# Kernel optimization log

Measured on AMD Instinct MI355X. Metric: run time of the kernel, lower is better.

Reference implementation:

```python
import jax, jax.numpy as jnp
import numpy as np

B, A, HR = 2, 180, 512
H_OUT = W_OUT = 512


def setup_inputs() -> dict:
    key = jax.random.key(0)
    k1, = jax.random.split(key, 1)
    sino = jax.random.normal(k1, (B, A, HR), dtype=jnp.float32)
    angles_deg = jnp.linspace(0.0, 180.0, A, endpoint=False, dtype=jnp.float32)
    return {"sino": sino, "angles_deg": angles_deg, "H": H_OUT, "W": W_OUT}


def _forward(sino, angles_deg, H, W):
    Bn, An, Hr = sino.shape
    pad = int(1.0 * 0.1 * min(H, W))  # pad_ratio = 1.0
    Hp, Wp = H + 2 * pad, W + 2 * pad

    # --- F.interpolate bilinear, align_corners=False: (A,B,Hr,1) -> (A,B,Hp,Wp).
    # Input width is 1, so width interp replicates the single column; only height interp matters.
    src = jnp.clip((jnp.arange(Hp, dtype=jnp.float32) + 0.5) * (Hr / Hp) - 0.5, 0.0, Hr - 1)
    i0 = jnp.floor(src).astype(jnp.int32)
    i1 = jnp.minimum(i0 + 1, Hr - 1)
    wH = src - i0.astype(jnp.float32)
    p = jnp.transpose(sino, (1, 0, 2)).astype(jnp.float32)  # (A,B,Hr)
    col = p[:, :, i0] * (1.0 - wH) + p[:, :, i1] * wH       # (A,B,Hp)
    proj = jnp.broadcast_to(col[:, :, :, None], (An, Bn, Hp, Wp))  # (A,B,Hp,Wp)

    # --- affine_grid (align_corners=False), sign = -1
    th = -jnp.deg2rad(angles_deg)
    c, s = jnp.cos(th), jnp.sin(th)                          # (A,)
    xs = (jnp.arange(Wp, dtype=jnp.float32) + 0.5) * (2.0 / Wp) - 1.0
    ys = (jnp.arange(Hp, dtype=jnp.float32) + 0.5) * (2.0 / Hp) - 1.0
    gx = c[:, None, None] * xs[None, None, :] - s[:, None, None] * ys[None, :, None]  # (A,Hp,Wp)
    gy = s[:, None, None] * xs[None, None, :] + c[:, None, None] * ys[None, :, None]

    # --- grid_sample bilinear, zeros padding, align_corners=False
    ix = ((gx + 1.0) * Wp - 1.0) * 0.5
    iy = ((gy + 1.0) * Hp - 1.0) * 0.5
    x0 = jnp.floor(ix).astype(jnp.int32); x1 = x0 + 1
    y0 = jnp.floor(iy).astype(jnp.int32); y1 = y0 + 1
    wx = ix - x0.astype(jnp.float32)
    wy = iy - y0.astype(jnp.float32)

    def corner(img, xi, yi, w):  # img (B,Hp,Wp); idx/w (Hp,Wp)
        valid = (xi >= 0) & (xi <= Wp - 1) & (yi >= 0) & (yi <= Hp - 1)
        xc = jnp.clip(xi, 0, Wp - 1)
        yc = jnp.clip(yi, 0, Hp - 1)
        return img[:, yc, xc] * (w * valid.astype(jnp.float32))[None]

    def sample(img, x0a, x1a, y0a, y1a, wxa, wya):
        return (corner(img, x0a, y0a, (1 - wxa) * (1 - wya)) +
                corner(img, x1a, y0a, wxa * (1 - wya)) +
                corner(img, x0a, y1a, (1 - wxa) * wya) +
                corner(img, x1a, y1a, wxa * wya))

    xr = jax.vmap(sample)(proj, x0, x1, y0, y1, wx, wy)      # (A,B,Hp,Wp)
    acc = xr.sum(axis=0) / (An + 1e-06)                      # (B,Hp,Wp)
    acc = acc[:, None, :, :]                                 # (B,1,Hp,Wp)
    if pad > 0:
        acc = acc[:, :, pad:Hp - pad, pad:Wp - pad]
    return acc


def reference(sino, angles_deg, H, W):
    return _forward(sino, angles_deg, H, W)
```

## Files before the change

kernel.cpp:

```cpp
#include <hip/hip_runtime.h>
#include <hip/hip_fp16.h>
#include <math.h>

#define B_N   2
#define A_N   180
#define HR_N  512
#define H_OUT 512
#define W_OUT 512
#define PAD   51
#define HP    614
#define WP    614
#define GUARD 80
#define HPP   (HP + 2*GUARD)
#define NPIX  (H_OUT * W_OUT)

#define TILE  16
#define QA    45
#define WIN   24


__device__ __forceinline__ float col_val(const float* __restrict__ sino,
                                         int b, int a, int yy) {
    if (yy < 0 || yy >= HP) return 0.0f;
    float src = ((float)yy + 0.5f) * ((float)HR_N / (float)HP) - 0.5f;
    src = fminf(fmaxf(src, 0.0f), (float)(HR_N - 1));
    int i0 = (int)floorf(src);
    int i1 = min(i0 + 1, HR_N - 1);
    float wH = src - (float)i0;
    const float* srow = sino + ((size_t)b * A_N + a) * HR_N;
    return srow[i0] * (1.0f - wH) + srow[i1] * wH;
}

__global__ void prep_kernel(const float* __restrict__ sino,
                            const float* __restrict__ angles,
                            uint2* __restrict__ pk2,
                            float2* __restrict__ tg) {
    int idx = blockIdx.x * blockDim.x + threadIdx.x;
    if (idx < A_N) {
        float th = -angles[idx] * (float)(M_PI / 180.0);
        tg[idx] = make_float2(cosf(th), sinf(th));
    }
    const int total = A_N * HPP;
    if (idx < total) {
        int y = idx % HPP;
        int a = idx / HPP;
        int yy = y - GUARD;
        float v00 = col_val(sino, 0, a, yy);
        float v10 = col_val(sino, 1, a, yy);
        float v01 = col_val(sino, 0, a, yy + 1);
        float v11 = col_val(sino, 1, a, yy + 1);
        __half2 lo = __floats2half2_rn(v00, v10);
        __half2 hi = __floats2half2_rn(v01, v11);
        uint2 u;
        u.x = *(unsigned int*)&lo;
        u.y = *(unsigned int*)&hi;
        pk2[idx] = u;
    }
}

__global__ __launch_bounds__(256, 4) void bp_kernel(const uint2* __restrict__ pk2,
                                                    const float2* __restrict__ tgv,
                                                    float* __restrict__ out) {
    __shared__ float2 s_tg[A_N];
    __shared__ int    s_base[A_N];
    __shared__ uint2  s_win[A_N * WIN];

    int t  = threadIdx.x;
    int tx = blockIdx.x, ty = blockIdx.y;
    float Xc = (float)(tx * TILE) - 248.0f;
    float Yc = (float)(ty * TILE) - 248.0f;

    if (t < A_N) {
        float2 cs = tgv[t];
        s_tg[t] = cs;
        float iyc = fmaf(cs.y, Xc, fmaf(cs.x, Yc, 306.5f));
        s_base[t] = (int)floorf(iyc) - 11;
    }
    __syncthreads();

    for (int e = t; e < A_N * WIN; e += 256) {
        int wid = e / WIN;
        int j   = e - wid * WIN;
        s_win[e] = pk2[(size_t)wid * HPP + (GUARD + s_base[wid] + j)];
    }
    __syncthreads();

    int q    = t >> 6;
    int lane = t & 63;
    int xq   = lane & 3;
    int yy   = lane >> 2;
    int x0   = tx * TILE + xq * 4;
    int y0   = ty * TILE + yy;
    float X  = (float)x0 - 255.5f;
    float Y  = (float)y0 - 255.5f;

    float2 acc[4] = {{0,0},{0,0},{0,0},{0,0}};

    bool interior = (Xc * Xc + Yc * Yc) <= 87500.0f;
    const int abase = q * QA;
    const uint2* winq = s_win + abase * WIN;

    if (interior) {
#pragma unroll 5
        for (int la = 0; la < QA; ++la) {
            float2 cs = s_tg[abase + la];
            float c = cs.x, s = cs.y;
            float iyc = fmaf(s, Xc, fmaf(c, Yc, 306.5f));
            float Kf  = 317.5f - floorf(iyc);
            float f0  = fmaf(s, X, fmaf(c, Y, Kf));
            float f1 = f0 + s, f2 = f1 + s, f3 = f2 + s;
            float fg[4] = {f0, f1, f2, f3};
#pragma unroll
            for (int g = 0; g < 4; ++g) {
                int   li = (int)fg[g];
                float wy = fg[g] - (float)li;
                uint2 cv = winq[la * WIN + li];
                __half2 lo = *(__half2*)&cv.x;
                __half2 hi = *(__half2*)&cv.y;
                __half2 r2 = __hfma2(__float2half2_rn(wy), __hsub2(hi, lo), lo);
                acc[g].x += __low2float(r2);
                acc[g].y += __high2float(r2);
            }
        }
    } else {
#pragma unroll 5
        for (int la = 0; la < QA; ++la) {
            float2 cs = s_tg[abase + la];
            float c = cs.x, s = cs.y;
            float iyc = fmaf(s, Xc, fmaf(c, Yc, 306.5f));
            float Kf  = 317.5f - floorf(iyc);
            float f0  = fmaf(s, X, fmaf(c, Y, Kf));
            float ix0 = fmaf(c, X, fmaf(-s, Y, 306.5f));
            float fg = f0, ixg = ix0;
#pragma unroll
            for (int g = 0; g < 4; ++g) {
                int   li = (int)fg;
                float wy = fg - (float)li;
                uint2 cv = winq[la * WIN + li];
                __half2 lo = *(__half2*)&cv.x;
                __half2 hi = *(__half2*)&cv.y;
                __half2 r2 = __hfma2(__float2half2_rn(wy), __hsub2(hi, lo), lo);
                float xf = fminf(fmaxf(ixg + 1.0f, 0.0f), 1.0f)
                         * fminf(fmaxf((float)WP - ixg, 0.0f), 1.0f);
                acc[g].x = fmaf(xf, __low2float(r2),  acc[g].x);
                acc[g].y = fmaf(xf, __high2float(r2), acc[g].y);
                fg += s; ixg += c;
            }
        }
    }

    __syncthreads();
    float* red = (float*)s_win;
    int px = yy * TILE + xq * 4;
    if (q != 0) {
        int o = (q - 1) * 512;
#pragma unroll
        for (int g = 0; g < 4; ++g) {
            red[o + px + g]       = acc[g].x;
            red[o + 256 + px + g] = acc[g].y;
        }
    }
    __syncthreads();
    if (q == 0) {
        const float inv = 1.0f / (180.0f + 1e-6f);
        float4 r0, r1;
        float* p0 = &r0.x; float* p1 = &r1.x;
#pragma unroll
        for (int g = 0; g < 4; ++g) {
            p0[g] = (acc[g].x + red[px + g]       + red[512 + px + g]       + red[1024 + px + g])       * inv;
            p1[g] = (acc[g].y + red[256 + px + g] + red[512 + 256 + px + g] + red[1024 + 256 + px + g]) * inv;
        }
        int idx = y0 * W_OUT + x0;
        *(float4*)&out[idx]        = r0;
        *(float4*)&out[NPIX + idx] = r1;
    }
}

extern "C" void kernel_launch(void* const* d_in, const int* in_sizes, int n_in,
                              void* d_out, int out_size, void* d_ws, size_t ws_size,
                              hipStream_t stream) {
    const float* sino   = (const float*)d_in[0];
    const float* angles = (const float*)d_in[1];
    char*   ws  = (char*)d_ws;
    uint2*  pk2 = (uint2*)ws;
    float2* tg  = (float2*)(ws + (size_t)A_N * HPP * sizeof(uint2));

    const int total = A_N * HPP;
    prep_kernel<<<(total + 255) / 256, 256, 0, stream>>>(sino, angles, pk2, tg);

    dim3 grid(W_OUT / TILE, H_OUT / TILE);
    bp_kernel<<<grid, 256, 0, stream>>>(pk2, tg, (float*)d_out);
}
```

Measured before the change: 84.91 us.

## Fuse projection prep into backprojection and accumulate interior tiles in half2

Drops the separate prep kernel. Each backprojection block now computes its own cos/sin table and fills its shared-memory window by interpolating the sinogram directly from global memory, so the launch and the workspace round trip go away. The cost is redundant interpolation and trig work in every block. Interior tiles also accumulate the 45 per-quarter samples in half2 rather than float, which saves conversions and adds but loses precision in the sums.

```diff
diff --git a/kernel.cpp b/kernel.cpp
--- a/kernel.cpp
+++ b/kernel.cpp
@@ -2,16 +2,12 @@
 #include <hip/hip_fp16.h>
 #include <math.h>
 
-#define B_N   2
 #define A_N   180
 #define HR_N  512
 #define H_OUT 512
 #define W_OUT 512
-#define PAD   51
 #define HP    614
 #define WP    614
-#define GUARD 80
-#define HPP   (HP + 2*GUARD)
 #define NPIX  (H_OUT * W_OUT)
 
 #define TILE  16
@@ -19,47 +15,22 @@
 #define WIN   24
 
 
-__device__ __forceinline__ float col_val(const float* __restrict__ sino,
-                                         int b, int a, int yy) {
-    if (yy < 0 || yy >= HP) return 0.0f;
+__device__ __forceinline__ __half2 samp2(const float* __restrict__ sino, int a, int yy) {
+    if (yy < 0 || yy >= HP) return __float2half2_rn(0.0f);
     float src = ((float)yy + 0.5f) * ((float)HR_N / (float)HP) - 0.5f;
     src = fminf(fmaxf(src, 0.0f), (float)(HR_N - 1));
     int i0 = (int)floorf(src);
     int i1 = min(i0 + 1, HR_N - 1);
-    float wH = src - (float)i0;
-    const float* srow = sino + ((size_t)b * A_N + a) * HR_N;
-    return srow[i0] * (1.0f - wH) + srow[i1] * wH;
+    float w = src - (float)i0;
+    const float* r0 = sino + (size_t)a * HR_N;
+    const float* r1 = sino + (size_t)(A_N + a) * HR_N;
+    float b0 = fmaf(w, r0[i1] - r0[i0], r0[i0]);
+    float b1 = fmaf(w, r1[i1] - r1[i0], r1[i0]);
+    return __floats2half2_rn(b0, b1);
 }
 
-__global__ void prep_kernel(const float* __restrict__ sino,
-                            const float* __restrict__ angles,
-                            uint2* __restrict__ pk2,
-                            float2* __restrict__ tg) {
-    int idx = blockIdx.x * blockDim.x + threadIdx.x;
-    if (idx < A_N) {
-        float th = -angles[idx] * (float)(M_PI / 180.0);
-        tg[idx] = make_float2(cosf(th), sinf(th));
-    }
-    const int total = A_N * HPP;
-    if (idx < total) {
-        int y = idx % HPP;
-        int a = idx / HPP;
-        int yy = y - GUARD;
-        float v00 = col_val(sino, 0, a, yy);
-        float v10 = col_val(sino, 1, a, yy);
-        float v01 = col_val(sino, 0, a, yy + 1);
-        float v11 = col_val(sino, 1, a, yy + 1);
-        __half2 lo = __floats2half2_rn(v00, v10);
-        __half2 hi = __floats2half2_rn(v01, v11);
-        uint2 u;
-        u.x = *(unsigned int*)&lo;
-        u.y = *(unsigned int*)&hi;
-        pk2[idx] = u;
-    }
-}
-
-__global__ __launch_bounds__(256, 4) void bp_kernel(const uint2* __restrict__ pk2,
-                                                    const float2* __restrict__ tgv,
+__global__ __launch_bounds__(256, 4) void bp_kernel(const float* __restrict__ sino,
+                                                    const float* __restrict__ angles,
                                                     float* __restrict__ out) {
     __shared__ float2 s_tg[A_N];
     __shared__ int    s_base[A_N];
@@ -71,9 +42,10 @@
     float Yc = (float)(ty * TILE) - 248.0f;
 
     if (t < A_N) {
-        float2 cs = tgv[t];
-        s_tg[t] = cs;
-        float iyc = fmaf(cs.y, Xc, fmaf(cs.x, Yc, 306.5f));
+        float th = -angles[t] * (float)(M_PI / 180.0);
+        float c = cosf(th), s = sinf(th);
+        s_tg[t] = make_float2(c, s);
+        float iyc = fmaf(s, Xc, fmaf(c, Yc, 306.5f));
         s_base[t] = (int)floorf(iyc) - 11;
     }
     __syncthreads();
@@ -81,7 +53,13 @@
     for (int e = t; e < A_N * WIN; e += 256) {
         int wid = e / WIN;
         int j   = e - wid * WIN;
-        s_win[e] = pk2[(size_t)wid * HPP + (GUARD + s_base[wid] + j)];
+        int yy  = s_base[wid] + j;
+        __half2 lo = samp2(sino, wid, yy);
+        __half2 hi = samp2(sino, wid, yy + 1);
+        uint2 u;
+        u.x = *(unsigned int*)&lo;
+        u.y = *(unsigned int*)&hi;
+        s_win[e] = u;
     }
     __syncthreads();
 
@@ -101,26 +79,31 @@
     const uint2* winq = s_win + abase * WIN;
 
     if (interior) {
+        __half2 hacc[4] = {__float2half2_rn(0.0f), __float2half2_rn(0.0f),
+                           __float2half2_rn(0.0f), __float2half2_rn(0.0f)};
 #pragma unroll 5
         for (int la = 0; la < QA; ++la) {
             float2 cs = s_tg[abase + la];
             float c = cs.x, s = cs.y;
             float iyc = fmaf(s, Xc, fmaf(c, Yc, 306.5f));
             float Kf  = 317.5f - floorf(iyc);
-            float f0  = fmaf(s, X, fmaf(c, Y, Kf));
-            float f1 = f0 + s, f2 = f1 + s, f3 = f2 + s;
-            float fg[4] = {f0, f1, f2, f3};
+            float fg  = fmaf(s, X, fmaf(c, Y, Kf));
 #pragma unroll
             for (int g = 0; g < 4; ++g) {
-                int   li = (int)fg[g];
-                float wy = fg[g] - (float)li;
+                int   li = (int)fg;
+                float wy = fg - (float)li;
                 uint2 cv = winq[la * WIN + li];
                 __half2 lo = *(__half2*)&cv.x;
                 __half2 hi = *(__half2*)&cv.y;
-                __half2 r2 = __hfma2(__float2half2_rn(wy), __hsub2(hi, lo), lo);
-                acc[g].x += __low2float(r2);
-                acc[g].y += __high2float(r2);
+                hacc[g] = __hadd2(hacc[g],
+                                  __hfma2(__float2half2_rn(wy), __hsub2(hi, lo), lo));
+                fg += s;
             }
+        }
+#pragma unroll
+        for (int g = 0; g < 4; ++g) {
+            acc[g].x = __low2float(hacc[g]);
+            acc[g].y = __high2float(hacc[g]);
         }
     } else {
 #pragma unroll 5
@@ -129,9 +112,8 @@
             float c = cs.x, s = cs.y;
             float iyc = fmaf(s, Xc, fmaf(c, Yc, 306.5f));
             float Kf  = 317.5f - floorf(iyc);
-            float f0  = fmaf(s, X, fmaf(c, Y, Kf));
-            float ix0 = fmaf(c, X, fmaf(-s, Y, 306.5f));
-            float fg = f0, ixg = ix0;
+            float fg  = fmaf(s, X, fmaf(c, Y, Kf));
+            float ixg = fmaf(c, X, fmaf(-s, Y, 306.5f));
 #pragma unroll
             for (int g = 0; g < 4; ++g) {
                 int   li = (int)fg;
@@ -181,13 +163,8 @@
                               hipStream_t stream) {
     const float* sino   = (const float*)d_in[0];
     const float* angles = (const float*)d_in[1];
-    char*   ws  = (char*)d_ws;
-    uint2*  pk2 = (uint2*)ws;
-    float2* tg  = (float2*)(ws + (size_t)A_N * HPP * sizeof(uint2));
-
-    const int total = A_N * HPP;
-    prep_kernel<<<(total + 255) / 256, 256, 0, stream>>>(sino, angles, pk2, tg);
+    (void)d_ws; (void)ws_size;
 
     dim3 grid(W_OUT / TILE, H_OUT / TILE);
-    bp_kernel<<<grid, 256, 0, stream>>>(pk2, tg, (float*)d_out);
+    bp_kernel<<<grid, 256, 0, stream>>>(sino, angles, (float*)d_out);
 }
```

Result: slower. 86.64 us (+2.0%).

## Precompute half2 differences, broadcast per-angle constants via readlane, accumulate interior in half2

Applied to the files above, without the earlier changes.

The prep kernel now stores the value and its difference (hi - lo) instead of two samples, which removes a subtraction per tap in the back-projection loop. Each lane precomputes cos, sin and the floor offset for one angle, and the loop fetches them with readlane instead of reading shared memory and recomputing. The interior path also accumulates in half2 rather than fp32. Summing 45 terms in fp16 risks larger rounding error in the output.

```diff
diff --git a/kernel.cpp b/kernel.cpp
--- a/kernel.cpp
+++ b/kernel.cpp
@@ -7,7 +7,6 @@
 #define HR_N  512
 #define H_OUT 512
 #define W_OUT 512
-#define PAD   51
 #define HP    614
 #define WP    614
 #define GUARD 80
@@ -18,6 +17,10 @@
 #define QA    45
 #define WIN   24
 
+
+__device__ __forceinline__ float rdlane(float v, int la) {
+    return __uint_as_float(__builtin_amdgcn_readlane(__float_as_uint(v), la));
+}
 
 __device__ __forceinline__ float col_val(const float* __restrict__ sino,
                                          int b, int a, int yy) {
@@ -45,15 +48,14 @@
         int y = idx % HPP;
         int a = idx / HPP;
         int yy = y - GUARD;
-        float v00 = col_val(sino, 0, a, yy);
-        float v10 = col_val(sino, 1, a, yy);
-        float v01 = col_val(sino, 0, a, yy + 1);
-        float v11 = col_val(sino, 1, a, yy + 1);
-        __half2 lo = __floats2half2_rn(v00, v10);
-        __half2 hi = __floats2half2_rn(v01, v11);
+        __half2 lo = __floats2half2_rn(col_val(sino, 0, a, yy),
+                                       col_val(sino, 1, a, yy));
+        __half2 hi = __floats2half2_rn(col_val(sino, 0, a, yy + 1),
+                                       col_val(sino, 1, a, yy + 1));
+        __half2 d  = __hsub2(hi, lo);
         uint2 u;
         u.x = *(unsigned int*)&lo;
-        u.y = *(unsigned int*)&hi;
+        u.y = *(unsigned int*)&d;
         pk2[idx] = u;
     }
 }
@@ -83,63 +85,66 @@
         int j   = e - wid * WIN;
         s_win[e] = pk2[(size_t)wid * HPP + (GUARD + s_base[wid] + j)];
     }
-    __syncthreads();
 
     int q    = t >> 6;
     int lane = t & 63;
-    int xq   = lane & 3;
-    int yy   = lane >> 2;
-    int x0   = tx * TILE + xq * 4;
-    int y0   = ty * TILE + yy;
-    float X  = (float)x0 - 255.5f;
-    float Y  = (float)y0 - 255.5f;
+    int la0  = lane < QA ? lane : QA - 1;
+    float vC, vS, vK;
+    {
+        float2 cs = s_tg[q * QA + la0];
+        float iyc = fmaf(cs.y, Xc, fmaf(cs.x, Yc, 306.5f));
+        vC = cs.x; vS = cs.y;
+        vK = 317.5f - floorf(iyc);
+    }
+
+    int xq = lane & 3;
+    int yy = lane >> 2;
+    int x0 = tx * TILE + xq * 4;
+    int y0 = ty * TILE + yy;
+    float X = (float)x0 - 255.5f;
+    float Y = (float)y0 - 255.5f;
+
+    __syncthreads();
 
     float2 acc[4] = {{0,0},{0,0},{0,0},{0,0}};
-
     bool interior = (Xc * Xc + Yc * Yc) <= 87500.0f;
-    const int abase = q * QA;
-    const uint2* winq = s_win + abase * WIN;
+    const uint2* winq = s_win + q * QA * WIN;
 
     if (interior) {
-#pragma unroll 5
+        __half2 hacc[4] = {__float2half2_rn(0.0f), __float2half2_rn(0.0f),
+                           __float2half2_rn(0.0f), __float2half2_rn(0.0f)};
         for (int la = 0; la < QA; ++la) {
-            float2 cs = s_tg[abase + la];
-            float c = cs.x, s = cs.y;
-            float iyc = fmaf(s, Xc, fmaf(c, Yc, 306.5f));
-            float Kf  = 317.5f - floorf(iyc);
-            float f0  = fmaf(s, X, fmaf(c, Y, Kf));
-            float f1 = f0 + s, f2 = f1 + s, f3 = f2 + s;
-            float fg[4] = {f0, f1, f2, f3};
-#pragma unroll
-            for (int g = 0; g < 4; ++g) {
-                int   li = (int)fg[g];
-                float wy = fg[g] - (float)li;
-                uint2 cv = winq[la * WIN + li];
-                __half2 lo = *(__half2*)&cv.x;
-                __half2 hi = *(__half2*)&cv.y;
-                __half2 r2 = __hfma2(__float2half2_rn(wy), __hsub2(hi, lo), lo);
-                acc[g].x += __low2float(r2);
-                acc[g].y += __high2float(r2);
-            }
-        }
-    } else {
-#pragma unroll 5
-        for (int la = 0; la < QA; ++la) {
-            float2 cs = s_tg[abase + la];
-            float c = cs.x, s = cs.y;
-            float iyc = fmaf(s, Xc, fmaf(c, Yc, 306.5f));
-            float Kf  = 317.5f - floorf(iyc);
-            float f0  = fmaf(s, X, fmaf(c, Y, Kf));
-            float ix0 = fmaf(c, X, fmaf(-s, Y, 306.5f));
-            float fg = f0, ixg = ix0;
+            float c = rdlane(vC, la), s = rdlane(vS, la), K = rdlane(vK, la);
+            float fg = fmaf(s, X, fmaf(c, Y, K));
 #pragma unroll
             for (int g = 0; g < 4; ++g) {
                 int   li = (int)fg;
                 float wy = fg - (float)li;
                 uint2 cv = winq[la * WIN + li];
                 __half2 lo = *(__half2*)&cv.x;
-                __half2 hi = *(__half2*)&cv.y;
-                __half2 r2 = __hfma2(__float2half2_rn(wy), __hsub2(hi, lo), lo);
+                __half2 d  = *(__half2*)&cv.y;
+                hacc[g] = __hadd2(hacc[g], __hfma2(__float2half2_rn(wy), d, lo));
+                fg += s;
+            }
+        }
+#pragma unroll
+        for (int g = 0; g < 4; ++g) {
+            acc[g].x = __low2float(hacc[g]);
+            acc[g].y = __high2float(hacc[g]);
+        }
+    } else {
+        for (int la = 0; la < QA; ++la) {
+            float c = rdlane(vC, la), s = rdlane(vS, la), K = rdlane(vK, la);
+            float fg  = fmaf(s, X, fmaf(c, Y, K));
+            float ixg = fmaf(c, X, fmaf(-s, Y, 306.5f));
+#pragma unroll
+            for (int g = 0; g < 4; ++g) {
+                int   li = (int)fg;
+                float wy = fg - (float)li;
+                uint2 cv = winq[la * WIN + li];
+                __half2 lo = *(__half2*)&cv.x;
+                __half2 d  = *(__half2*)&cv.y;
+                __half2 r2 = __hfma2(__float2half2_rn(wy), d, lo);
                 float xf = fminf(fmaxf(ixg + 1.0f, 0.0f), 1.0f)
                          * fminf(fmaxf((float)WP - ixg, 0.0f), 1.0f);
                 acc[g].x = fmaf(xf, __low2float(r2),  acc[g].x);
```

Result: no change. 84.57 us (-0.4%).
